# Optimization experiments

Measured on AMD Instinct MI355X. Metric: run time of the kernel, lower is better.

The kernel has to match this reference:

```python
import jax, jax.numpy as jnp
import numpy as np

THRESHOLD = 0.5
NEG_POS_RATIO = 3
ALPHA = 1.0
B, A, C, M = 128, 8732, 21, 8


def cxcy_to_xy(c):
    return jnp.concatenate([c[:, :2] - c[:, 2:] / 2.0, c[:, :2] + c[:, 2:] / 2.0], axis=1)


def cxcy_to_gcxgcy(cxcy, priors):
    g_cxcy = (cxcy[:, :2] - priors[:, :2]) / (priors[:, 2:] / 10.0)
    g_wh = jnp.log(cxcy[:, 2:] / priors[:, 2:]) * 5.0
    return jnp.concatenate([g_cxcy, g_wh], axis=1)


def find_jaccard_overlap(a, b):
    # a: [M,4] xy, b: [A,4] xy -> IoU [M,A]
    lt = jnp.maximum(a[:, None, :2], b[None, :, :2])
    rb = jnp.minimum(a[:, None, 2:], b[None, :, 2:])
    wh = jnp.clip(rb - lt, 0.0)
    inter = wh[..., 0] * wh[..., 1]
    area_a = (a[:, 2] - a[:, 0]) * (a[:, 3] - a[:, 1])
    area_b = (b[:, 2] - b[:, 0]) * (b[:, 3] - b[:, 1])
    return inter / (area_a[:, None] + area_b[None, :] - inter)


def setup_inputs() -> dict:
    key = jax.random.key(0)
    k1, k2, k3, k4, k5, k6 = jax.random.split(key, 6)
    predicted_locs = jax.random.normal(k1, (B, A, 4), dtype=jnp.float32)
    predicted_scores = jax.random.normal(k2, (B, A, C), dtype=jnp.float32)
    # ground-truth boxes in xy pixel coords within [0, 300], guaranteed x2>x1, y2>y1
    u = jax.random.uniform(k3, (B, M, 4), dtype=jnp.float32)
    x1y1 = u[..., :2] * 150.0
    x2y2 = x1y1 + u[..., 2:] * 140.0 + 10.0
    boxes = jnp.concatenate([x1y1, x2y2], axis=-1)
    labels = jax.random.randint(k4, (B, M), 1, C)  # 1..20, never background
    # anchor boxes in cxcy, w/h strictly positive
    cxcy = jax.random.uniform(k5, (A, 2), dtype=jnp.float32)
    wh = 0.05 + 0.95 * jax.random.uniform(k6, (A, 2), dtype=jnp.float32)
    anchor_boxes = jnp.concatenate([cxcy, wh], axis=1)
    return {"predicted_locs": predicted_locs, "predicted_scores": predicted_scores,
            "boxes": boxes, "labels": labels, "anchor_boxes": anchor_boxes}


def _match(boxes_i, labels_i, anchors_cxcy, anchors_xy):
    # boxes_i: [M,4] xy pixels, labels_i: [M]
    scaled = boxes_i / 300.0
    iou = find_jaccard_overlap(scaled, anchors_xy)            # [M, A]
    obj_for_anchor = jnp.argmax(iou, axis=0)                  # [A]
    iou_for_anchor = jnp.max(iou, axis=0)                     # [A]
    anchor_for_obj = jnp.argmax(iou, axis=1)                  # [M]
    obj_for_anchor = obj_for_anchor.at[anchor_for_obj].set(jnp.arange(M))
    iou_for_anchor = iou_for_anchor.at[anchor_for_obj].set(1.0)
    label_for_anchor = labels_i[obj_for_anchor]               # [A]
    label_for_anchor = jnp.where(iou_for_anchor < THRESHOLD, 0, label_for_anchor)
    true_locs = cxcy_to_gcxgcy(boxes_i[obj_for_anchor], anchors_cxcy)  # [A,4]
    return label_for_anchor, true_locs


def reference(predicted_locs, predicted_scores, boxes, labels, anchor_boxes):
    anchors_xy = cxcy_to_xy(anchor_boxes)
    true_classes, true_locs = jax.vmap(_match, in_axes=(0, 0, None, None))(
        boxes, labels, anchor_boxes, anchors_xy)              # [B,A], [B,A,4]

    pos = true_classes != 0                                   # [B,A]
    n_pos = pos.sum(axis=1)                                   # [B]
    n_pos_total = n_pos.sum()

    # L1Loss(mean) over positive anchors' 4 coords
    l1 = jnp.abs(predicted_locs - true_locs)                  # [B,A,4]
    loc_loss = (l1 * pos[..., None]).sum() / (n_pos_total.astype(jnp.float32) * 4.0)

    # per-anchor cross entropy
    logp = jax.nn.log_softmax(predicted_scores, axis=-1)      # [B,A,C]
    ce = -jnp.take_along_axis(logp, true_classes[..., None], axis=-1)[..., 0]  # [B,A]

    conf_pos = (ce * pos).sum()
    ce_neg = jnp.where(pos, 0.0, ce)
    ce_neg_sorted = -jnp.sort(-ce_neg, axis=1)                # descending per row
    ranks = jnp.arange(A)[None, :]
    hard = ranks < (NEG_POS_RATIO * n_pos)[:, None]
    conf_hard_neg = (ce_neg_sorted * hard).sum()

    conf_loss = (conf_hard_neg + conf_pos) / n_pos_total.astype(jnp.float32)
    return conf_loss + ALPHA * loc_loss
```

## Files before the change

kernel.cpp:

```cpp
#include <hip/hip_runtime.h>
#include <hip/hip_bf16.h>

constexpr int B = 128;
constexpr int A = 8732;
constexpr int C = 21;
constexpr int M = 8;

__global__ void k_init(float* accf, int* npt) {
    int t = threadIdx.x;
    if (t < 3) accf[t] = 0.f;
    if (t == 3) *npt = 0;
}

__global__ __launch_bounds__(1024) void k_match(
    const float* __restrict__ boxes,
    const int*   __restrict__ labels,
    const float* __restrict__ anchors,
    int*         __restrict__ packed,
    int*         __restrict__ n_pos,
    int*         __restrict__ npt)
{
    __shared__ float         s_iou[A];
    __shared__ unsigned char s_obj[A];
    __shared__ float s_pv[M][16];
    __shared__ int   s_pi[M][16];
    __shared__ int   s_force[M];
    __shared__ int   s_c[16];
    __shared__ float s_box[M][4];
    __shared__ int   s_lab[M];

    const int b = blockIdx.x;
    const int t = threadIdx.x;
    const int lane = t & 63;
    const int wv   = t >> 6;

    if (t < M * 4) ((float*)s_box)[t] = boxes[b * M * 4 + t];
    if (t < M)     s_lab[t] = labels[b * M + t];
    __syncthreads();

    float bb[M][4], barea[M];
#pragma unroll
    for (int m = 0; m < M; m++) {
        bb[m][0] = s_box[m][0] / 300.f;
        bb[m][1] = s_box[m][1] / 300.f;
        bb[m][2] = s_box[m][2] / 300.f;
        bb[m][3] = s_box[m][3] / 300.f;
        barea[m] = (bb[m][2] - bb[m][0]) * (bb[m][3] - bb[m][1]);
    }

    float bestv[M];
    int   besti[M];
#pragma unroll
    for (int m = 0; m < M; m++) { bestv[m] = -1.f; besti[m] = 0; }

    const float4* anch4 = (const float4*)anchors;
    for (int a = t; a < A; a += 1024) {
        float4 an = anch4[a];
        float ax1 = an.x - an.z / 2.0f, ay1 = an.y - an.w / 2.0f;
        float ax2 = an.x + an.z / 2.0f, ay2 = an.y + an.w / 2.0f;
        float aarea = (ax2 - ax1) * (ay2 - ay1);

        float bmax = -1.f; int bm = 0;
#pragma unroll
        for (int m = 0; m < M; m++) {
            float lx = fmaxf(bb[m][0], ax1), ly = fmaxf(bb[m][1], ay1);
            float rx = fminf(bb[m][2], ax2), ry = fminf(bb[m][3], ay2);
            float iw = fmaxf(rx - lx, 0.f), ih = fmaxf(ry - ly, 0.f);
            float inter = iw * ih;
            float iou = inter / (barea[m] + aarea - inter);
            if (iou > bmax) { bmax = iou; bm = m; }
            if (iou > bestv[m]) { bestv[m] = iou; besti[m] = a; }
        }
        s_iou[a] = bmax;
        s_obj[a] = (unsigned char)bm;
    }

#pragma unroll
    for (int m = 0; m < M; m++) {
        float v = bestv[m]; int i = besti[m];
        for (int off = 32; off > 0; off >>= 1) {
            float ov = __shfl_down(v, off);
            int   oi = __shfl_down(i, off);
            if (ov > v || (ov == v && oi < i)) { v = ov; i = oi; }
        }
        if (lane == 0) { s_pv[m][wv] = v; s_pi[m][wv] = i; }
    }
    __syncthreads();

    if (t < M) {
        float bv = -1.f; int bi = 0x7fffffff;
#pragma unroll
        for (int w = 0; w < 16; w++) {
            float v = s_pv[t][w]; int i = s_pi[t][w];
            if (v > bv || (v == bv && i < bi)) { bv = v; bi = i; }
        }
        s_force[t] = bi;
    }
    __syncthreads();

    if (t == 0) {
        for (int m = 0; m < M; m++) {
            int a = s_force[m];
            s_obj[a] = (unsigned char)m;
            s_iou[a] = 1.0f;
        }
    }
    __syncthreads();

    int cnt = 0;
    for (int a = t; a < A; a += 1024) {
        int obj = s_obj[a];
        int lab = s_lab[obj];
        if (s_iou[a] < 0.5f) lab = 0;
        packed[(size_t)b * A + a] = lab | (obj << 8);
        if (lab != 0) cnt++;
    }
    for (int off = 32; off > 0; off >>= 1) cnt += __shfl_down(cnt, off);
    if (lane == 0) s_c[wv] = cnt;
    __syncthreads();
    if (t == 0) {
        int c0 = 0;
#pragma unroll
        for (int w = 0; w < 16; w++) c0 += s_c[w];
        n_pos[b] = c0;
        atomicAdd(npt, c0);
    }
}

__global__ __launch_bounds__(256) void k_ce(
    const float* __restrict__ plocs,
    const float* __restrict__ pscores,
    const float* __restrict__ boxes,
    const float* __restrict__ anchors,
    int*         __restrict__ buf,
    float*       __restrict__ accf)
{
    constexpr int NQ = B * A / 4;
    const int i4 = blockIdx.x * 256 + threadIdx.x;
    float l_pos = 0.f, l_loc = 0.f;

    if (i4 < NQ) {
        const int base = i4 * 4;
        const float4* s4 = (const float4*)(pscores + (size_t)base * C);
        float4 v[21];
#pragma unroll
        for (int i = 0; i < 21; i++) v[i] = s4[i];
        const float* f = (const float*)v;

        int4 pk4 = ((const int4*)buf)[i4];
        const int pks[4] = {pk4.x, pk4.y, pk4.z, pk4.w};

        const int b = base / A;
        const int a0 = base - b * A;

        float4 cn4;
        float* cn = (float*)&cn4;
#pragma unroll
        for (int j = 0; j < 4; j++) {
            const float* row = f + j * C;
            const int lab = pks[j] & 255;
            const int obj = pks[j] >> 8;

            float mx = row[0];
#pragma unroll
            for (int c = 1; c < C; c++) mx = fmaxf(mx, row[c]);
            float sum = 0.f, slab = 0.f;
#pragma unroll
            for (int c = 0; c < C; c++) {
                sum += __expf(row[c] - mx);
                if (c == lab) slab = row[c];
            }
            float ce = mx + __logf(sum) - slab;

            cn[j] = ce;
            if (lab != 0) {
                cn[j] = 0.f;
                l_pos += ce;
                const float* bx = boxes + ((size_t)b * M + obj) * 4;
                const float* an = anchors + (size_t)(a0 + j) * 4;
                float dx = (bx[0] - an[0]) / (an[2] / 10.f);
                float dy = (bx[1] - an[1]) / (an[3] / 10.f);
                float dw = logf(bx[2] / an[2]) * 5.f;
                float dh = logf(bx[3] / an[3]) * 5.f;
                float4 p = ((const float4*)plocs)[base + j];
                l_loc += fabsf(p.x - dx) + fabsf(p.y - dy) +
                         fabsf(p.z - dw) + fabsf(p.w - dh);
            }
        }
        ((float4*)buf)[i4] = cn4;
    }

    for (int off = 32; off > 0; off >>= 1) {
        l_pos += __shfl_down(l_pos, off);
        l_loc += __shfl_down(l_loc, off);
    }
    if ((threadIdx.x & 63) == 0 && (l_pos != 0.f || l_loc != 0.f)) {
        atomicAdd(&accf[0], l_pos);
        atomicAdd(&accf[1], l_loc);
    }
}

__global__ __launch_bounds__(1024) void k_topk(
    const float* __restrict__ ce_neg,
    const int*   __restrict__ n_pos,
    float*       __restrict__ accf)
{
    __shared__ unsigned int vals[A];
    __shared__ unsigned int hist[256];
    __shared__ unsigned int s_prefix, s_krem;
    __shared__ float        rs[16];
    __shared__ unsigned int rc[16];

    const int b = blockIdx.x;
    const int t = threadIdx.x;
    const int lane = t & 63;
    const int wv   = t >> 6;
    const int K = 3 * n_pos[b];
    const float* row = ce_neg + (size_t)b * A;

    {
        const uint4* r4 = (const uint4*)row;
        uint4* v4 = (uint4*)vals;
        for (int i = t; i < A / 4; i += 1024) v4[i] = r4[i];
    }
    if (t == 0) { s_prefix = 0u; s_krem = (unsigned)K; }
    __syncthreads();

    if (K <= 0) return;

    if (K >= A) {
        float s = 0.f;
        for (int i = t; i < A; i += 1024) s += __uint_as_float(vals[i]);
        for (int off = 32; off > 0; off >>= 1) s += __shfl_down(s, off);
        if (lane == 0) rs[wv] = s;
        __syncthreads();
        if (t == 0) {
            float tot = 0.f;
#pragma unroll
            for (int w = 0; w < 16; w++) tot += rs[w];
            atomicAdd(&accf[2], tot);
        }
        return;
    }

    for (int pass = 0; pass < 4; pass++) {
        const int shift = 24 - 8 * pass;
        const unsigned pref = s_prefix;
        const unsigned krem = s_krem;
        if (t < 256) hist[t] = 0u;
        __syncthreads();
        for (int i = t; i < A; i += 1024) {
            unsigned int v = vals[i];
            if (pass == 0 || (v >> (shift + 8)) == pref)
                atomicAdd(&hist[(v >> shift) & 255u], 1u);
        }
        __syncthreads();
        if (t < 64) {
            unsigned h0 = hist[4 * t + 0], h1 = hist[4 * t + 1];
            unsigned h2 = hist[4 * t + 2], h3 = hist[4 * t + 3];
            unsigned s3 = h3, s2 = h2 + s3, s1 = h1 + s2, s0 = h0 + s1;
            unsigned suf = s0;
            for (int off = 1; off < 64; off <<= 1) {
                unsigned o = __shfl_down(suf, off);
                if (t + off < 64) suf += o;
            }
            unsigned above = suf - s0;
            hist[4 * t + 0] = above + s0;
            hist[4 * t + 1] = above + s1;
            hist[4 * t + 2] = above + s2;
            hist[4 * t + 3] = above + s3;
        }
        __syncthreads();
        if (t < 256) {
            unsigned ssT = hist[t];
            unsigned ssN = (t < 255) ? hist[t + 1] : 0u;
            if (ssT >= krem && ssN < krem) {
                s_prefix = (pref << 8) | (unsigned)t;
                s_krem   = krem - ssN;
            }
        }
        __syncthreads();
    }

    const unsigned int tb = s_prefix;
    float sg = 0.f; unsigned int cg = 0;
    for (int i = t; i < A; i += 1024) {
        unsigned int v = vals[i];
        if (v > tb) { sg += __uint_as_float(v); cg++; }
    }
    for (int off = 32; off > 0; off >>= 1) {
        sg += __shfl_down(sg, off);
        cg += __shfl_down(cg, off);
    }
    if (lane == 0) { rs[wv] = sg; rc[wv] = cg; }
    __syncthreads();
    if (t == 0) {
        float tv = __uint_as_float(tb);
        float tot = 0.f; unsigned cnt = 0;
#pragma unroll
        for (int w = 0; w < 16; w++) { tot += rs[w]; cnt += rc[w]; }
        atomicAdd(&accf[2], tot + (float)(K - (int)cnt) * tv);
    }
}

__global__ void k_final(const float* __restrict__ accf,
                        const int* __restrict__ npt,
                        float* __restrict__ out)
{
    float n = (float)(*npt);
    float conf_loss = (accf[2] + accf[0]) / n;
    float loc_loss  = accf[1] / (n * 4.f);
    out[0] = conf_loss + loc_loss;
}

extern "C" void kernel_launch(void* const* d_in, const int* in_sizes, int n_in,
                              void* d_out, int out_size, void* d_ws, size_t ws_size,
                              hipStream_t stream)
{
    const float* plocs   = (const float*)d_in[0];
    const float* pscores = (const float*)d_in[1];
    const float* boxes   = (const float*)d_in[2];
    const int*   labels  = (const int*)d_in[3];
    const float* anchors = (const float*)d_in[4];
    float*       out     = (float*)d_out;

    float* accf  = (float*)d_ws;
    int*   npt   = (int*)d_ws + 3;
    int*   n_pos = (int*)d_ws + 8;
    int*   buf   = (int*)d_ws + 8 + B;

    k_init<<<1, 64, 0, stream>>>(accf, npt);
    k_match<<<B, 1024, 0, stream>>>(boxes, labels, anchors, buf, n_pos, npt);
    constexpr int NQ = B * A / 4;
    k_ce<<<(NQ + 255) / 256, 256, 0, stream>>>(plocs, pscores, boxes, anchors, buf, accf);
    k_topk<<<B, 1024, 0, stream>>>((const float*)buf, n_pos, accf);
    k_final<<<1, 1, 0, stream>>>(accf, npt, out);
}
```

Before: 287.8 us.

## Fuse loc loss into match, split CE across thread pairs, bisect top-k threshold

```diff
diff --git a/kernel.cpp b/kernel.cpp
--- a/kernel.cpp
+++ b/kernel.cpp
@@ -1,24 +1,20 @@
 #include <hip/hip_runtime.h>
-#include <hip/hip_bf16.h>
 
 constexpr int B = 128;
 constexpr int A = 8732;
 constexpr int C = 21;
 constexpr int M = 8;
 
-__global__ void k_init(float* accf, int* npt) {
-    int t = threadIdx.x;
-    if (t < 3) accf[t] = 0.f;
-    if (t == 3) *npt = 0;
-}
 
 __global__ __launch_bounds__(1024) void k_match(
     const float* __restrict__ boxes,
     const int*   __restrict__ labels,
     const float* __restrict__ anchors,
+    const float* __restrict__ plocs,
     int*         __restrict__ packed,
-    int*         __restrict__ n_pos,
-    int*         __restrict__ npt)
+    int*         __restrict__ row_npos,
+    float*       __restrict__ row_loc,
+    float*       __restrict__ accf)
 {
     __shared__ float         s_iou[A];
     __shared__ unsigned char s_obj[A];
@@ -26,6 +22,7 @@
     __shared__ int   s_pi[M][16];
     __shared__ int   s_force[M];
     __shared__ int   s_c[16];
+    __shared__ float s_l[16];
     __shared__ float s_box[M][4];
     __shared__ int   s_lab[M];
 
@@ -107,115 +104,126 @@
     }
     __syncthreads();
 
-    int cnt = 0;
+    int cnt = 0; float lloc = 0.f;
     for (int a = t; a < A; a += 1024) {
         int obj = s_obj[a];
-        int lab = s_lab[obj];
-        if (s_iou[a] < 0.5f) lab = 0;
-        packed[(size_t)b * A + a] = lab | (obj << 8);
-        if (lab != 0) cnt++;
-    }
-    for (int off = 32; off > 0; off >>= 1) cnt += __shfl_down(cnt, off);
-    if (lane == 0) s_c[wv] = cnt;
+        int lab = (s_iou[a] < 0.5f) ? 0 : s_lab[obj];
+        packed[(size_t)b * A + a] = lab;
+        if (lab != 0) {
+            cnt++;
+            float4 an = anch4[a];
+            const float* bx = s_box[obj];
+            float dx = (bx[0] - an.x) / (an.z / 10.f);
+            float dy = (bx[1] - an.y) / (an.w / 10.f);
+            float dw = logf(bx[2] / an.z) * 5.f;
+            float dh = logf(bx[3] / an.w) * 5.f;
+            float4 p = ((const float4*)plocs)[(size_t)b * A + a];
+            lloc += fabsf(p.x - dx) + fabsf(p.y - dy) +
+                    fabsf(p.z - dw) + fabsf(p.w - dh);
+        }
+    }
+    for (int off = 32; off > 0; off >>= 1) {
+        cnt  += __shfl_down(cnt, off);
+        lloc += __shfl_down(lloc, off);
+    }
+    if (lane == 0) { s_c[wv] = cnt; s_l[wv] = lloc; }
     __syncthreads();
     if (t == 0) {
-        int c0 = 0;
-#pragma unroll
-        for (int w = 0; w < 16; w++) c0 += s_c[w];
-        n_pos[b] = c0;
-        atomicAdd(npt, c0);
-    }
-}
-
-__global__ __launch_bounds__(256) void k_ce(
-    const float* __restrict__ plocs,
+        int tc = 0; float tl = 0.f;
+#pragma unroll
+        for (int w = 0; w < 16; w++) { tc += s_c[w]; tl += s_l[w]; }
+        row_npos[b] = tc;
+        row_loc[b]  = tl;
+        if (b == 0) accf[0] = 0.f;
+    }
+}
+
+__global__ __launch_bounds__(256, 4) void k_ce(
     const float* __restrict__ pscores,
-    const float* __restrict__ boxes,
-    const float* __restrict__ anchors,
     int*         __restrict__ buf,
     float*       __restrict__ accf)
 {
-    constexpr int NQ = B * A / 4;
-    const int i4 = blockIdx.x * 256 + threadIdx.x;
-    float l_pos = 0.f, l_loc = 0.f;
-
-    if (i4 < NQ) {
-        const int base = i4 * 4;
-        const float4* s4 = (const float4*)(pscores + (size_t)base * C);
-        float4 v[21];
-#pragma unroll
-        for (int i = 0; i < 21; i++) v[i] = s4[i];
-        const float* f = (const float*)v;
-
-        int4 pk4 = ((const int4*)buf)[i4];
-        const int pks[4] = {pk4.x, pk4.y, pk4.z, pk4.w};
-
-        const int b = base / A;
-        const int a0 = base - b * A;
-
-        float4 cn4;
-        float* cn = (float*)&cn4;
-#pragma unroll
-        for (int j = 0; j < 4; j++) {
-            const float* row = f + j * C;
-            const int lab = pks[j] & 255;
-            const int obj = pks[j] >> 8;
-
-            float mx = row[0];
-#pragma unroll
-            for (int c = 1; c < C; c++) mx = fmaxf(mx, row[c]);
-            float sum = 0.f, slab = 0.f;
-#pragma unroll
-            for (int c = 0; c < C; c++) {
-                sum += __expf(row[c] - mx);
-                if (c == lab) slab = row[c];
+    const int tid = blockIdx.x * 256 + threadIdx.x;
+    const int q = tid >> 1;
+    const int h = tid & 1;
+    const float4* sp = (const float4*)pscores + (size_t)q * 21;
+
+    float4 r[11];
+    if (h == 0) {
+#pragma unroll
+        for (int j = 0; j < 11; j++) r[j] = sp[j];
+    } else {
+#pragma unroll
+        for (int j = 0; j < 10; j++) r[j] = sp[11 + j];
+    }
+    const int4 pk4 = ((const int4*)buf)[q];
+    const int labs[4] = {pk4.x, pk4.y, pk4.z, pk4.w};
+
+    float sum[4] = {0.f, 0.f, 0.f, 0.f};
+    float sel[4] = {0.f, 0.f, 0.f, 0.f};
+
+    if (h == 0) {
+#pragma unroll
+        for (int j = 0; j < 11; j++) {
+            const float vv[4] = {r[j].x, r[j].y, r[j].z, r[j].w};
+#pragma unroll
+            for (int e = 0; e < 4; e++) {
+                const int fi = j * 4 + e;
+                const int al = fi / 21, c = fi % 21;
+                sum[al] += __expf(vv[e]);
+                if (c == labs[al]) sel[al] = vv[e];
             }
-            float ce = mx + __logf(sum) - slab;
-
-            cn[j] = ce;
-            if (lab != 0) {
-                cn[j] = 0.f;
-                l_pos += ce;
-                const float* bx = boxes + ((size_t)b * M + obj) * 4;
-                const float* an = anchors + (size_t)(a0 + j) * 4;
-                float dx = (bx[0] - an[0]) / (an[2] / 10.f);
-                float dy = (bx[1] - an[1]) / (an[3] / 10.f);
-                float dw = logf(bx[2] / an[2]) * 5.f;
-                float dh = logf(bx[3] / an[3]) * 5.f;
-                float4 p = ((const float4*)plocs)[base + j];
-                l_loc += fabsf(p.x - dx) + fabsf(p.y - dy) +
-                         fabsf(p.z - dw) + fabsf(p.w - dh);
+        }
+    } else {
+#pragma unroll
+        for (int j = 0; j < 10; j++) {
+            const float vv[4] = {r[j].x, r[j].y, r[j].z, r[j].w};
+#pragma unroll
+            for (int e = 0; e < 4; e++) {
+                const int fi = 44 + j * 4 + e;
+                const int al = fi / 21, c = fi % 21;
+                sum[al] += __expf(vv[e]);
+                if (c == labs[al]) sel[al] = vv[e];
             }
         }
-        ((float4*)buf)[i4] = cn4;
-    }
-
-    for (int off = 32; off > 0; off >>= 1) {
-        l_pos += __shfl_down(l_pos, off);
-        l_loc += __shfl_down(l_loc, off);
-    }
-    if ((threadIdx.x & 63) == 0 && (l_pos != 0.f || l_loc != 0.f)) {
-        atomicAdd(&accf[0], l_pos);
-        atomicAdd(&accf[1], l_loc);
-    }
+    }
+#pragma unroll
+    for (int al = 0; al < 4; al++) {
+        sum[al] += __shfl_xor(sum[al], 1);
+        sel[al] += __shfl_xor(sel[al], 1);
+    }
+
+    float l_pos = 0.f;
+    if (h == 0) {
+        float4 cn;
+        float* cnp = (float*)&cn;
+#pragma unroll
+        for (int al = 0; al < 4; al++) {
+            float ce = __logf(sum[al]) - sel[al];
+            ce = fmaxf(ce, 0.f);
+            if (labs[al] != 0) { l_pos += ce; ce = 0.f; }
+            cnp[al] = ce;
+        }
+        ((float4*)buf)[q] = cn;
+    }
+    for (int off = 32; off > 0; off >>= 1) l_pos += __shfl_down(l_pos, off);
+    if ((threadIdx.x & 63) == 0 && l_pos != 0.f) atomicAdd(&accf[0], l_pos);
 }
 
 __global__ __launch_bounds__(1024) void k_topk(
     const float* __restrict__ ce_neg,
-    const int*   __restrict__ n_pos,
-    float*       __restrict__ accf)
-{
-    __shared__ unsigned int vals[A];
-    __shared__ unsigned int hist[256];
-    __shared__ unsigned int s_prefix, s_krem;
-    __shared__ float        rs[16];
-    __shared__ unsigned int rc[16];
+    const int*   __restrict__ row_npos,
+    float*       __restrict__ row_hard)
+{
+    __shared__ unsigned vals[A];
+    __shared__ unsigned s_u[16];
+    __shared__ float    s_f[16];
 
     const int b = blockIdx.x;
     const int t = threadIdx.x;
     const int lane = t & 63;
     const int wv   = t >> 6;
-    const int K = 3 * n_pos[b];
+    const int K = 3 * row_npos[b];
     const float* row = ce_neg + (size_t)b * A;
 
     {
@@ -223,94 +231,89 @@
         uint4* v4 = (uint4*)vals;
         for (int i = t; i < A / 4; i += 1024) v4[i] = r4[i];
     }
-    if (t == 0) { s_prefix = 0u; s_krem = (unsigned)K; }
-    __syncthreads();
-
-    if (K <= 0) return;
+    __syncthreads();
+
+    if (K <= 0) { if (t == 0) row_hard[b] = 0.f; return; }
 
     if (K >= A) {
         float s = 0.f;
         for (int i = t; i < A; i += 1024) s += __uint_as_float(vals[i]);
         for (int off = 32; off > 0; off >>= 1) s += __shfl_down(s, off);
-        if (lane == 0) rs[wv] = s;
+        if (lane == 0) s_f[wv] = s;
         __syncthreads();
         if (t == 0) {
             float tot = 0.f;
 #pragma unroll
-            for (int w = 0; w < 16; w++) tot += rs[w];
-            atomicAdd(&accf[2], tot);
+            for (int w = 0; w < 16; w++) tot += s_f[w];
+            row_hard[b] = tot;
         }
         return;
     }
 
-    for (int pass = 0; pass < 4; pass++) {
-        const int shift = 24 - 8 * pass;
-        const unsigned pref = s_prefix;
-        const unsigned krem = s_krem;
-        if (t < 256) hist[t] = 0u;
+    unsigned lo = 0u, hi = 0x7F800000u;
+    while (lo < hi) {
+        const unsigned mid = lo + ((hi - lo) >> 1);
+        int cnt = 0;
+        for (int i = t; i < A; i += 1024) cnt += (vals[i] > mid) ? 1 : 0;
+        for (int off = 32; off > 0; off >>= 1) cnt += __shfl_down(cnt, off);
+        if (lane == 0) s_u[wv] = (unsigned)cnt;
         __syncthreads();
-        for (int i = t; i < A; i += 1024) {
-            unsigned int v = vals[i];
-            if (pass == 0 || (v >> (shift + 8)) == pref)
-                atomicAdd(&hist[(v >> shift) & 255u], 1u);
-        }
+        int tot = 0;
+#pragma unroll
+        for (int w = 0; w < 16; w++) tot += (int)s_u[w];
+        if (tot < K) hi = mid; else lo = mid + 1;
         __syncthreads();
-        if (t < 64) {
-            unsigned h0 = hist[4 * t + 0], h1 = hist[4 * t + 1];
-            unsigned h2 = hist[4 * t + 2], h3 = hist[4 * t + 3];
-            unsigned s3 = h3, s2 = h2 + s3, s1 = h1 + s2, s0 = h0 + s1;
-            unsigned suf = s0;
-            for (int off = 1; off < 64; off <<= 1) {
-                unsigned o = __shfl_down(suf, off);
-                if (t + off < 64) suf += o;
-            }
-            unsigned above = suf - s0;
-            hist[4 * t + 0] = above + s0;
-            hist[4 * t + 1] = above + s1;
-            hist[4 * t + 2] = above + s2;
-            hist[4 * t + 3] = above + s3;
-        }
-        __syncthreads();
-        if (t < 256) {
-            unsigned ssT = hist[t];
-            unsigned ssN = (t < 255) ? hist[t + 1] : 0u;
-            if (ssT >= krem && ssN < krem) {
-                s_prefix = (pref << 8) | (unsigned)t;
-                s_krem   = krem - ssN;
-            }
-        }
-        __syncthreads();
-    }
-
-    const unsigned int tb = s_prefix;
-    float sg = 0.f; unsigned int cg = 0;
+    }
+    const unsigned tb = lo;
+
+    float sg = 0.f; int cg = 0;
     for (int i = t; i < A; i += 1024) {
-        unsigned int v = vals[i];
+        unsigned v = vals[i];
         if (v > tb) { sg += __uint_as_float(v); cg++; }
     }
     for (int off = 32; off > 0; off >>= 1) {
         sg += __shfl_down(sg, off);
         cg += __shfl_down(cg, off);
     }
-    if (lane == 0) { rs[wv] = sg; rc[wv] = cg; }
+    if (lane == 0) { s_f[wv] = sg; s_u[wv] = (unsigned)cg; }
     __syncthreads();
     if (t == 0) {
-        float tv = __uint_as_float(tb);
-        float tot = 0.f; unsigned cnt = 0;
-#pragma unroll
-        for (int w = 0; w < 16; w++) { tot += rs[w]; cnt += rc[w]; }
-        atomicAdd(&accf[2], tot + (float)(K - (int)cnt) * tv);
-    }
-}
-
-__global__ void k_final(const float* __restrict__ accf,
-                        const int* __restrict__ npt,
-                        float* __restrict__ out)
-{
-    float n = (float)(*npt);
-    float conf_loss = (accf[2] + accf[0]) / n;
-    float loc_loss  = accf[1] / (n * 4.f);
-    out[0] = conf_loss + loc_loss;
+        float tot = 0.f; int cnt = 0;
+#pragma unroll
+        for (int w = 0; w < 16; w++) { tot += s_f[w]; cnt += (int)s_u[w]; }
+        row_hard[b] = tot + (float)(K - cnt) * __uint_as_float(tb);
+    }
+}
+
+__global__ __launch_bounds__(128) void k_final(
+    const float* __restrict__ accf,
+    const int*   __restrict__ row_npos,
+    const float* __restrict__ row_loc,
+    const float* __restrict__ row_hard,
+    float*       __restrict__ out)
+{
+    __shared__ int   s_n[2];
+    __shared__ float s_l[2], s_h[2];
+    const int t = threadIdx.x;
+    const int lane = t & 63;
+    const int wv = t >> 6;
+
+    int np = row_npos[t];
+    float lc = row_loc[t];
+    float hd = row_hard[t];
+    for (int off = 32; off > 0; off >>= 1) {
+        np += __shfl_down(np, off);
+        lc += __shfl_down(lc, off);
+        hd += __shfl_down(hd, off);
+    }
+    if (lane == 0) { s_n[wv] = np; s_l[wv] = lc; s_h[wv] = hd; }
+    __syncthreads();
+    if (t == 0) {
+        float n = (float)(s_n[0] + s_n[1]);
+        float conf = (accf[0] + s_h[0] + s_h[1]) / n;
+        float loc  = (s_l[0] + s_l[1]) / (n * 4.f);
+        out[0] = conf + loc;
+    }
 }
 
 extern "C" void kernel_launch(void* const* d_in, const int* in_sizes, int n_in,
@@ -324,15 +327,15 @@
     const float* anchors = (const float*)d_in[4];
     float*       out     = (float*)d_out;
 
-    float* accf  = (float*)d_ws;
-    int*   npt   = (int*)d_ws + 3;
-    int*   n_pos = (int*)d_ws + 8;
-    int*   buf   = (int*)d_ws + 8 + B;
-
-    k_init<<<1, 64, 0, stream>>>(accf, npt);
-    k_match<<<B, 1024, 0, stream>>>(boxes, labels, anchors, buf, n_pos, npt);
-    constexpr int NQ = B * A / 4;
-    k_ce<<<(NQ + 255) / 256, 256, 0, stream>>>(plocs, pscores, boxes, anchors, buf, accf);
-    k_topk<<<B, 1024, 0, stream>>>((const float*)buf, n_pos, accf);
-    k_final<<<1, 1, 0, stream>>>(accf, npt, out);
-}
+    float* accf     = (float*)d_ws;
+    int*   row_npos = (int*)d_ws + 8;
+    float* row_loc  = (float*)d_ws + 136;
+    float* row_hard = (float*)d_ws + 264;
+    int*   buf      = (int*)d_ws + 392;
+
+    k_match<<<B, 1024, 0, stream>>>(boxes, labels, anchors, plocs,
+                                    buf, row_npos, row_loc, accf);
+    k_ce<<<(B * A / 2) / 256, 256, 0, stream>>>(pscores, buf, accf);
+    k_topk<<<B, 1024, 0, stream>>>((const float*)buf, row_npos, row_hard);
+    k_final<<<1, 128, 0, stream>>>(accf, row_npos, row_loc, row_hard, out);
+}
```

Measured after the change: 292.0 us. No clear change (+1.5%).
